# Performance work log

Hardware: AMD Instinct MI355X
Metric: run time of the kernel (lower is better)

## Reference

```python
import jax, jax.numpy as jnp
import numpy as np

# ---- static config (from search_space / module defaults) ----
B, NCG = 4096, 2                 # batch of archs, cell groups
NUM_INIT, NUM_NODE_INPUTS, NUM_STEPS = 2, 2, 4
NUM_NODES = NUM_INIT + NUM_STEPS  # 6
N_EDGE = NUM_NODE_INPUTS * NUM_STEPS  # 8
NUM_OPS = 7                      # 'none' is index 0
NONE_INDEX = 0
NODE_DIM = OP_DIM = HIDDEN = 48
GCN_DIMS = [128, 128]


def _uniform(key, shape, fan_in):
    s = 1.0 / np.sqrt(fan_in)
    return jax.random.uniform(key, shape, minval=-s, maxval=s, dtype=jnp.float32)


def setup_inputs() -> dict:
    key = jax.random.key(0)
    ks = jax.random.split(key, 14)
    # from-node for step i must be < NUM_INIT + i -> per-edge maxval [2,2,3,3,4,4,5,5]
    fmax = jnp.repeat(jnp.arange(NUM_INIT, NUM_NODES), NUM_NODE_INPUTS)
    f_nodes = jax.random.randint(ks[0], (B, NCG, N_EDGE), 0, fmax)
    ops = jax.random.randint(ks[1], (B, NCG, N_EDGE), 0, NUM_OPS)
    archs = jnp.stack([f_nodes, ops], axis=2).astype(jnp.int32)  # (B,NCG,2,E)

    init_node_emb = jax.random.normal(ks[2], (NCG, NUM_INIT, NODE_DIM), dtype=jnp.float32)
    other_node_emb = jnp.zeros((NCG, 1, NODE_DIM), dtype=jnp.float32)  # zero-init, trainable
    # op embeddings; 'none' op (idx 0) is frozen zeros
    op_embs = jax.random.normal(ks[3], (NUM_OPS, OP_DIM), dtype=jnp.float32).at[NONE_INDEX].set(0.0)

    Wx = _uniform(ks[4], (NODE_DIM, HIDDEN), NODE_DIM)
    bx = _uniform(ks[5], (HIDDEN,), NODE_DIM)
    W1 = _uniform(ks[6], (HIDDEN, GCN_DIMS[0]), GCN_DIMS[0])
    Wa1 = _uniform(ks[7], (OP_DIM, GCN_DIMS[0]), OP_DIM)
    ba1 = _uniform(ks[8], (GCN_DIMS[0],), OP_DIM)
    W2 = _uniform(ks[9], (GCN_DIMS[0], GCN_DIMS[1]), GCN_DIMS[1])
    Wa2 = _uniform(ks[10], (OP_DIM, GCN_DIMS[1]), OP_DIM)
    ba2 = _uniform(ks[11], (GCN_DIMS[1],), OP_DIM)
    return {"archs": archs, "init_node_emb": init_node_emb, "other_node_emb": other_node_emb,
            "op_embs": op_embs, "Wx": Wx, "bx": bx, "W1": W1, "Wa1": Wa1, "ba1": ba1,
            "W2": W2, "Wa2": Wa2, "ba2": ba2}


def _build_adj_ops(archs):
    """Dense adjacency (edge counts) and per-input-slot op-index matrices."""
    f = archs[:, :, 0, :].reshape(-1, N_EDGE)    # (B*NCG, E) from-nodes
    ops = archs[:, :, 1, :].reshape(-1, N_EDGE)  # (B*NCG, E) op ids
    t = jnp.repeat(jnp.arange(NUM_INIT, NUM_NODES), NUM_NODE_INPUTS)  # (E,) to-nodes
    Bt = B * NCG
    b_idx = jnp.arange(Bt)[:, None]
    adj = jnp.zeros((Bt, NUM_NODES, NUM_NODES), jnp.float32)
    adj = adj.at[b_idx, t[None, :], f].add(1.0)
    adj_op_inds = []
    for k in range(NUM_NODE_INPUTS):
        fk, tk, opk = f[:, k::NUM_NODE_INPUTS], t[k::NUM_NODE_INPUTS], ops[:, k::NUM_NODE_INPUTS]
        aoi = jnp.full((Bt, NUM_NODES, NUM_NODES), NONE_INDEX, dtype=jnp.int32)
        aoi = aoi.at[b_idx, tk[None, :], fk].set(opk)  # (t,f) unique within a slot
        adj_op_inds.append(aoi.reshape(B, NCG, NUM_NODES, NUM_NODES))
    return adj.reshape(B, NCG, NUM_NODES, NUM_NODES), adj_op_inds


def _gcn_layer(y, adj_op_inds, op_embs, W, Wa, ba):
    """DenseGraphOpEdgeFlow (defaults: attention, no plus_I/normalize/bias):
    out_i = support_i + sum_slots sum_j sigmoid(att(op_emb[op_ij])) * 1[op_ij != none] * support_j
    """
    support = y @ W                                   # (B,CG,N,out)
    out = support
    for aoi in adj_op_inds:
        attn = jax.nn.sigmoid(op_embs[aoi] @ Wa + ba)  # (B,CG,N,N,out)
        attn = attn * (aoi != NONE_INDEX)[..., None].astype(support.dtype)
        out = out + jnp.einsum('bcijo,bcjo->bcio', attn, support)
    return out


def reference(archs, init_node_emb, other_node_emb, op_embs, Wx, bx,
              W1, Wa1, ba1, W2, Wa2, ba2):
    _adj, adj_op_inds = _build_adj_ops(archs)  # adj counts unused under default gcn_kwargs
    node = jnp.concatenate([
        jnp.broadcast_to(init_node_emb[None], (B, NCG, NUM_INIT, NODE_DIM)),
        jnp.broadcast_to(other_node_emb[None], (B, NCG, NUM_STEPS, NODE_DIM))], axis=2)
    y = node @ Wx + bx                                 # x_hidden
    y = _gcn_layer(y, adj_op_inds, op_embs, W1, Wa1, ba1)
    y = jax.nn.relu(y)                                 # relu between layers
    y = _gcn_layer(y, adj_op_inds, op_embs, W2, Wa2, ba2)
    y = y[:, :, NUM_INIT:, :].mean(axis=2)             # drop init nodes, mean over steps
    return y.reshape(B, -1)                            # (B, NCG*128)
```

## Files before the change

kernel.cpp:

```cpp
#include <hip/hip_runtime.h>

#define NPAIR 8192

#define WS_S1   0
#define WS_AT1  1536
#define WS_AT2  2432
#define WS_S2I  3328

__device__ __forceinline__ float sigmoidf_(float x) {
  return 1.0f / (1.0f + __expf(-x));
}

__global__ __launch_bounds__(512) void precompute_kernel(
    const float* __restrict__ init_emb, const float* __restrict__ other_emb,
    const float* __restrict__ op_embs,  const float* __restrict__ Wx,
    const float* __restrict__ bx,       const float* __restrict__ W1,
    const float* __restrict__ Wa1,      const float* __restrict__ ba1,
    const float* __restrict__ W2,       const float* __restrict__ Wa2,
    const float* __restrict__ ba2,      float* __restrict__ ws)
{
  const int t   = threadIdx.x;
  const int blk = blockIdx.x;

  __shared__ float y0[2 * 6 * 48];
  __shared__ float s1sh[2 * 6 * 128];

  for (int idx = t; idx < 2 * 6 * 48; idx += 512) {
    int c = idx / 288, i = (idx / 48) % 6, h = idx % 48;
    const float* nptr = (i < 2) ? (init_emb + (c * 2 + i) * 48)
                                : (other_emb + c * 48);
    float acc = bx[h];
    for (int d = 0; d < 48; ++d)
      acc += nptr[d] * Wx[d * 48 + h];
    y0[idx] = acc;
  }
  __syncthreads();

  for (int idx = t; idx < 2 * 6 * 128; idx += 512) {
    int ci = idx >> 7, o = idx & 127;
    const float* yp = y0 + ci * 48;
    float acc = 0.f;
    for (int h = 0; h < 48; ++h) acc += yp[h] * W1[h * 128 + o];
    s1sh[idx] = acc;
    ws[WS_S1 + idx] = acc;
  }

  for (int idx = blk * 112 + t; idx < (blk + 1) * 112; idx += 512) {
    int op = idx >> 7, o = idx & 127;
    float a1 = ba1[o], a2 = ba2[o];
    for (int d = 0; d < 48; ++d) {
      float e = op_embs[op * 48 + d];
      a1 += e * Wa1[d * 128 + o];
      a2 += e * Wa2[d * 128 + o];
    }
    ws[WS_AT1 + idx] = (op == 0) ? 0.f : sigmoidf_(a1);
    ws[WS_AT2 + idx] = (op == 0) ? 0.f : sigmoidf_(a2);
  }
  __syncthreads();

  for (int idx = blk * 64 + t; idx < (blk + 1) * 64; idx += 512) {
    int c = idx >> 8, i = (idx >> 7) & 1, o = idx & 127;
    const float* sp = s1sh + (c * 6 + i) * 128;
    float acc = 0.f;
    for (int h = 0; h < 128; ++h)
      acc += fmaxf(sp[h], 0.f) * W2[h * 128 + o];
    ws[WS_S2I + idx] = acc;
  }
}

#define COMP4(v, j) ((j) == 0 ? (v).x : (j) == 1 ? (v).y : (j) == 2 ? (v).z : (v).w)

__global__ __launch_bounds__(256) void main_kernel(
    const int* __restrict__ archs, const float* __restrict__ W2,
    const float* __restrict__ ws, float* __restrict__ out)
{
  const int t  = threadIdx.x;
  const int pp = t >> 6;
  const int o2 = t & 63;
  const int P  = blockIdx.x * 4 + pp;
  const int c  = P & 1;

  __shared__ float w2sh[8192];
  __shared__ float y1sh[4][512];
  __shared__ int   archsh[64];
  if (t < 64) archsh[t] = archs[blockIdx.x * 64 + t];
  __syncthreads();

  int f[8], op[8];
  #pragma unroll
  for (int e = 0; e < 8; ++e) { f[e] = archsh[pp * 16 + e]; op[e] = archsh[pp * 16 + 8 + e]; }

  const float2* s1p = (const float2*)ws + c * 384;
  const float2* at1 = (const float2*)(ws + WS_AT1);
  const float2* at2 = (const float2*)(ws + WS_AT2);
  const float2* s2i = (const float2*)(ws + WS_S2I) + c * 128;

  float2 A2[8];
  #pragma unroll
  for (int e = 0; e < 8; ++e) A2[e] = at2[op[e] * 64 + o2];
  float2 S0 = s2i[o2], S1 = s2i[64 + o2];

  #pragma unroll
  for (int i = 0; i < 4; ++i) {
    float2 v = s1p[(2 + i) * 64 + o2];
    int e0 = 2 * i, e1 = 2 * i + 1;
    float2 A0 = at1[op[e0] * 64 + o2];
    float2 B0 = s1p[f[e0] * 64 + o2];
    float2 A1 = at1[op[e1] * 64 + o2];
    float2 B1 = s1p[f[e1] * 64 + o2];
    v.x += A0.x * B0.x + A1.x * B1.x;
    v.y += A0.y * B0.y + A1.y * B1.y;
    ((float2*)(y1sh[pp] + i * 128))[o2] =
        make_float2(fmaxf(v.x, 0.f), fmaxf(v.y, 0.f));
  }

  const float* y1p = y1sh[pp];
  float ax0 = 0, ax1 = 0, ax2 = 0, ax3 = 0;
  float ay0 = 0, ay1 = 0, ay2 = 0, ay3 = 0;

  for (int half = 0; half < 2; ++half) {
    __syncthreads();
    #pragma unroll
    for (int k = 0; k < 8; ++k)
      ((float4*)w2sh)[t + k * 256] = ((const float4*)W2)[half * 2048 + t + k * 256];
    __syncthreads();

    const float2* w2f = (const float2*)w2sh;
    const float*  yh  = y1p + half * 64;
    for (int h = 0; h < 64; h += 4) {
      float4 q0 = *(const float4*)(yh + 0 * 128 + h);
      float4 q1 = *(const float4*)(yh + 1 * 128 + h);
      float4 q2 = *(const float4*)(yh + 2 * 128 + h);
      float4 q3 = *(const float4*)(yh + 3 * 128 + h);
      #pragma unroll
      for (int j = 0; j < 4; ++j) {
        float2 wf = w2f[(h + j) * 64 + o2];
        float w0 = wf.x, w1 = wf.y, y;
        y = COMP4(q0, j); ax0 += y * w0; ay0 += y * w1;
        y = COMP4(q1, j); ax1 += y * w0; ay1 += y * w1;
        y = COMP4(q2, j); ax2 += y * w0; ay2 += y * w1;
        y = COMP4(q3, j); ax3 += y * w0; ay3 += y * w1;
      }
    }
  }

  float r0 = ax0 + ax1 + ax2 + ax3;
  float r1 = ay0 + ay1 + ay2 + ay3;
  #pragma unroll
  for (int e = 0; e < 8; ++e) {
    int fe = f[e];
    float sx, sy;
    if (fe == 0)      { sx = S0.x; sy = S0.y; }
    else if (fe == 1) { sx = S1.x; sy = S1.y; }
    else if (fe == 2) { sx = ax0; sy = ay0; }
    else if (fe == 3) { sx = ax1; sy = ay1; }
    else if (fe == 4) { sx = ax2; sy = ay2; }
    else              { sx = ax3; sy = ay3; }
    r0 += A2[e].x * sx;
    r1 += A2[e].y * sy;
  }
  r0 *= 0.25f; r1 *= 0.25f;

  ((float2*)out)[P * 64 + o2] = make_float2(r0, r1);
}

extern "C" void kernel_launch(void* const* d_in, const int* in_sizes, int n_in,
                              void* d_out, int out_size, void* d_ws, size_t ws_size,
                              hipStream_t stream) {
  const int* archs = (const int*)d_in[0];
  float* ws = (float*)d_ws;
  precompute_kernel<<<8, 512, 0, stream>>>(
      (const float*)d_in[1], (const float*)d_in[2], (const float*)d_in[3],
      (const float*)d_in[4], (const float*)d_in[5], (const float*)d_in[6],
      (const float*)d_in[7], (const float*)d_in[8], (const float*)d_in[9],
      (const float*)d_in[10], (const float*)d_in[11], ws);
  main_kernel<<<NPAIR / 4, 256, 0, stream>>>(archs, (const float*)d_in[9], ws,
                                             (float*)d_out);
}
```

Baseline: 121.3 us.

## Precompute second-layer support for all node configurations and gather per arch

Each intermediate node's first-layer output depends only on its two (from-node, op) inputs and the cell group. The new path enumerates all 5292 possible configurations, computes their layer-2 support (y1 @ W2) once in a config kernel, and stores them in a workspace table. The per-arch kernel then only gathers four table rows plus the attention terms, removing the per-arch 128x128 matmul. The old path stays as a fallback when the workspace is too small, and it now reads W2 directly from global memory instead of staging it in shared memory.

```diff
diff --git a/kernel.cpp b/kernel.cpp
--- a/kernel.cpp
+++ b/kernel.cpp
@@ -2,14 +2,195 @@
 
 #define NPAIR 8192
 
-#define WS_S1   0
-#define WS_AT1  1536
-#define WS_AT2  2432
-#define WS_S2I  3328
+#define NCFG_REAL 5292
+#define NCFG      5296
+#define CPER      2646
+#define WS_AT2F   0
+#define WS_TAB    1024
+#define WS_NEED   ((size_t)(1024 + NCFG * 128) * 4)
+
+#define COMP4(v, j) ((j) == 0 ? (v).x : (j) == 1 ? (v).y : (j) == 2 ? (v).z : (v).w)
 
 __device__ __forceinline__ float sigmoidf_(float x) {
   return 1.0f / (1.0f + __expf(-x));
 }
+
+__global__ __launch_bounds__(512) void config_kernel(
+    const float* __restrict__ init_emb, const float* __restrict__ other_emb,
+    const float* __restrict__ op_embs,  const float* __restrict__ Wx,
+    const float* __restrict__ bx,       const float* __restrict__ W1,
+    const float* __restrict__ Wa1,      const float* __restrict__ ba1,
+    const float* __restrict__ W2,       const float* __restrict__ Wa2,
+    const float* __restrict__ ba2,      float* __restrict__ ws)
+{
+  __shared__ float y0[576];
+  __shared__ float s1sh[1536];
+  __shared__ float at1sh[896];
+  __shared__ float at2sh[896];
+  __shared__ float y1sh[8192];
+  const int t = threadIdx.x;
+
+  for (int idx = t; idx < 576; idx += 512) {
+    int c = idx / 288, i = (idx / 48) % 6, h = idx % 48;
+    const float* nptr = (i < 2) ? (init_emb + (c * 2 + i) * 48)
+                                : (other_emb + c * 48);
+    float acc = bx[h];
+    for (int d = 0; d < 48; ++d) acc += nptr[d] * Wx[d * 48 + h];
+    y0[idx] = acc;
+  }
+  for (int idx = t; idx < 896; idx += 512) {
+    int op = idx >> 7, o = idx & 127;
+    float a1 = ba1[o], a2 = ba2[o];
+    for (int d = 0; d < 48; ++d) {
+      float e = op_embs[op * 48 + d];
+      a1 += e * Wa1[d * 128 + o];
+      a2 += e * Wa2[d * 128 + o];
+    }
+    float v1 = (op == 0) ? 0.f : sigmoidf_(a1);
+    float v2 = (op == 0) ? 0.f : sigmoidf_(a2);
+    at1sh[idx] = v1;
+    at2sh[idx] = v2;
+    ws[WS_AT2F + idx] = v2;
+  }
+  __syncthreads();
+  for (int idx = t; idx < 1536; idx += 512) {
+    int ci = idx >> 7, o = idx & 127;
+    const float* yp = y0 + ci * 48;
+    float acc = 0.f;
+    for (int h = 0; h < 48; ++h) acc += yp[h] * W1[h * 128 + o];
+    s1sh[idx] = acc;
+  }
+  __syncthreads();
+
+  const int w  = t >> 6, o2 = t & 63;
+  const int cfg0 = (blockIdx.x * 8 + w) * 8;
+  const float2* s1f = (const float2*)s1sh;
+  const float2* a1f = (const float2*)at1sh;
+
+  #pragma unroll
+  for (int r = 0; r < 8; ++r) {
+    int cfg = cfg0 + r;
+    if (cfg >= NCFG) continue;
+    float2 v;
+    if (cfg < NCFG_REAL) {
+      int c = cfg / CPER, q = cfg % CPER;
+      int i, b;
+      if (q < 196)       { i = 2; b = 0; }
+      else if (q < 637)  { i = 3; b = 196; }
+      else if (q < 1421) { i = 4; b = 637; }
+      else               { i = 5; b = 1421; }
+      q -= b;
+      int op2_ = q % 7; q /= 7;
+      int f2_  = q % i; q /= i;
+      int op1_ = q % 7;
+      int f1_  = q / 7;
+      int cb = c * 384;
+      v = s1f[cb + i * 64 + o2];
+      float2 A0 = a1f[op1_ * 64 + o2], B0 = s1f[cb + f1_ * 64 + o2];
+      float2 A1 = a1f[op2_ * 64 + o2], B1 = s1f[cb + f2_ * 64 + o2];
+      v.x += A0.x * B0.x + A1.x * B1.x;
+      v.y += A0.y * B0.y + A1.y * B1.y;
+    } else {
+      int j = cfg - NCFG_REAL, c = j >> 1, i = j & 1;
+      v = s1f[c * 384 + i * 64 + o2];
+    }
+    ((float2*)(y1sh + (w * 8 + r) * 128))[o2] =
+        make_float2(fmaxf(v.x, 0.f), fmaxf(v.y, 0.f));
+  }
+  __syncthreads();
+
+  const float* yb = y1sh + (w * 8) * 128;
+  const float2* W2f = (const float2*)W2;
+  float2 acc[8];
+  #pragma unroll
+  for (int r = 0; r < 8; ++r) acc[r] = make_float2(0.f, 0.f);
+
+  for (int k = 0; k < 128; k += 4) {
+    float4 yv[8];
+    #pragma unroll
+    for (int r = 0; r < 8; ++r)
+      yv[r] = *(const float4*)(yb + r * 128 + k);
+    #pragma unroll
+    for (int j = 0; j < 4; ++j) {
+      float2 wv = W2f[(k + j) * 64 + o2];
+      #pragma unroll
+      for (int r = 0; r < 8; ++r) {
+        float y = COMP4(yv[r], j);
+        acc[r].x += y * wv.x;
+        acc[r].y += y * wv.y;
+      }
+    }
+  }
+
+  float2* tab = (float2*)(ws + WS_TAB);
+  #pragma unroll
+  for (int r = 0; r < 8; ++r) {
+    int cfg = cfg0 + r;
+    if (cfg < NCFG) tab[cfg * 64 + o2] = acc[r];
+  }
+}
+
+__global__ __launch_bounds__(256) void gather_kernel(
+    const int* __restrict__ archs, const float* __restrict__ ws,
+    float* __restrict__ out)
+{
+  const int t  = threadIdx.x;
+  const int pp = t >> 6;
+  const int o2 = t & 63;
+  const int P  = blockIdx.x * 4 + pp;
+  const int c  = P & 1;
+
+  __shared__ int archsh[64];
+  if (t < 64) archsh[t] = archs[blockIdx.x * 64 + t];
+  __syncthreads();
+
+  int f[8], op[8];
+  #pragma unroll
+  for (int e = 0; e < 8; ++e) { f[e] = archsh[pp * 16 + e]; op[e] = archsh[pp * 16 + 8 + e]; }
+
+  const float2* tab = (const float2*)(ws + WS_TAB);
+  const float2* a2f = (const float2*)(ws + WS_AT2F);
+
+  float2 S0 = tab[(NCFG_REAL + c * 2 + 0) * 64 + o2];
+  float2 S1 = tab[(NCFG_REAL + c * 2 + 1) * 64 + o2];
+  float2 S2, S3, S4, S5;
+  {
+    const int ib[4] = {0, 196, 637, 1421};
+    #pragma unroll
+    for (int i = 2; i < 6; ++i) {
+      int e0 = 2 * (i - 2), e1 = e0 + 1;
+      int cid = c * CPER + ib[i - 2] +
+                ((f[e0] * 7 + op[e0]) * i + f[e1]) * 7 + op[e1];
+      float2 v = tab[cid * 64 + o2];
+      if (i == 2) S2 = v; else if (i == 3) S3 = v;
+      else if (i == 4) S4 = v; else S5 = v;
+    }
+  }
+  float2 A2[8];
+  #pragma unroll
+  for (int e = 0; e < 8; ++e) A2[e] = a2f[op[e] * 64 + o2];
+
+  float r0 = S2.x + S3.x + S4.x + S5.x;
+  float r1 = S2.y + S3.y + S4.y + S5.y;
+  #pragma unroll
+  for (int e = 0; e < 8; ++e) {
+    int fe = f[e];
+    float sx, sy;
+    if (fe == 0)      { sx = S0.x; sy = S0.y; }
+    else if (fe == 1) { sx = S1.x; sy = S1.y; }
+    else if (fe == 2) { sx = S2.x; sy = S2.y; }
+    else if (fe == 3) { sx = S3.x; sy = S3.y; }
+    else              { sx = S4.x; sy = S4.y; }
+    r0 += A2[e].x * sx;
+    r1 += A2[e].y * sy;
+  }
+  ((float2*)out)[P * 64 + o2] = make_float2(r0 * 0.25f, r1 * 0.25f);
+}
+
+#define FB_S1   0
+#define FB_AT1  1536
+#define FB_AT2  2432
+#define FB_S2I  3328
 
 __global__ __launch_bounds__(512) void precompute_kernel(
     const float* __restrict__ init_emb, const float* __restrict__ other_emb,
@@ -21,30 +202,25 @@
 {
   const int t   = threadIdx.x;
   const int blk = blockIdx.x;
-
-  __shared__ float y0[2 * 6 * 48];
-  __shared__ float s1sh[2 * 6 * 128];
-
-  for (int idx = t; idx < 2 * 6 * 48; idx += 512) {
+  __shared__ float y0[576];
+  __shared__ float s1sh[1536];
+  for (int idx = t; idx < 576; idx += 512) {
     int c = idx / 288, i = (idx / 48) % 6, h = idx % 48;
     const float* nptr = (i < 2) ? (init_emb + (c * 2 + i) * 48)
                                 : (other_emb + c * 48);
     float acc = bx[h];
-    for (int d = 0; d < 48; ++d)
-      acc += nptr[d] * Wx[d * 48 + h];
+    for (int d = 0; d < 48; ++d) acc += nptr[d] * Wx[d * 48 + h];
     y0[idx] = acc;
   }
   __syncthreads();
-
-  for (int idx = t; idx < 2 * 6 * 128; idx += 512) {
+  for (int idx = t; idx < 1536; idx += 512) {
     int ci = idx >> 7, o = idx & 127;
     const float* yp = y0 + ci * 48;
     float acc = 0.f;
     for (int h = 0; h < 48; ++h) acc += yp[h] * W1[h * 128 + o];
     s1sh[idx] = acc;
-    ws[WS_S1 + idx] = acc;
-  }
-
+    ws[FB_S1 + idx] = acc;
+  }
   for (int idx = blk * 112 + t; idx < (blk + 1) * 112; idx += 512) {
     int op = idx >> 7, o = idx & 127;
     float a1 = ba1[o], a2 = ba2[o];
@@ -53,22 +229,18 @@
       a1 += e * Wa1[d * 128 + o];
       a2 += e * Wa2[d * 128 + o];
     }
-    ws[WS_AT1 + idx] = (op == 0) ? 0.f : sigmoidf_(a1);
-    ws[WS_AT2 + idx] = (op == 0) ? 0.f : sigmoidf_(a2);
-  }
-  __syncthreads();
-
+    ws[FB_AT1 + idx] = (op == 0) ? 0.f : sigmoidf_(a1);
+    ws[FB_AT2 + idx] = (op == 0) ? 0.f : sigmoidf_(a2);
+  }
+  __syncthreads();
   for (int idx = blk * 64 + t; idx < (blk + 1) * 64; idx += 512) {
     int c = idx >> 8, i = (idx >> 7) & 1, o = idx & 127;
     const float* sp = s1sh + (c * 6 + i) * 128;
     float acc = 0.f;
-    for (int h = 0; h < 128; ++h)
-      acc += fmaxf(sp[h], 0.f) * W2[h * 128 + o];
-    ws[WS_S2I + idx] = acc;
-  }
-}
-
-#define COMP4(v, j) ((j) == 0 ? (v).x : (j) == 1 ? (v).y : (j) == 2 ? (v).z : (v).w)
+    for (int h = 0; h < 128; ++h) acc += fmaxf(sp[h], 0.f) * W2[h * 128 + o];
+    ws[FB_S2I + idx] = acc;
+  }
+}
 
 __global__ __launch_bounds__(256) void main_kernel(
     const int* __restrict__ archs, const float* __restrict__ W2,
@@ -79,27 +251,21 @@
   const int o2 = t & 63;
   const int P  = blockIdx.x * 4 + pp;
   const int c  = P & 1;
-
-  __shared__ float w2sh[8192];
   __shared__ float y1sh[4][512];
   __shared__ int   archsh[64];
   if (t < 64) archsh[t] = archs[blockIdx.x * 64 + t];
   __syncthreads();
-
   int f[8], op[8];
   #pragma unroll
   for (int e = 0; e < 8; ++e) { f[e] = archsh[pp * 16 + e]; op[e] = archsh[pp * 16 + 8 + e]; }
-
   const float2* s1p = (const float2*)ws + c * 384;
-  const float2* at1 = (const float2*)(ws + WS_AT1);
-  const float2* at2 = (const float2*)(ws + WS_AT2);
-  const float2* s2i = (const float2*)(ws + WS_S2I) + c * 128;
-
+  const float2* at1 = (const float2*)(ws + FB_AT1);
+  const float2* at2 = (const float2*)(ws + FB_AT2);
+  const float2* s2i = (const float2*)(ws + FB_S2I) + c * 128;
   float2 A2[8];
   #pragma unroll
   for (int e = 0; e < 8; ++e) A2[e] = at2[op[e] * 64 + o2];
   float2 S0 = s2i[o2], S1 = s2i[64 + o2];
-
   #pragma unroll
   for (int i = 0; i < 4; ++i) {
     float2 v = s1p[(2 + i) * 64 + o2];
@@ -113,37 +279,26 @@
     ((float2*)(y1sh[pp] + i * 128))[o2] =
         make_float2(fmaxf(v.x, 0.f), fmaxf(v.y, 0.f));
   }
-
+  __syncthreads();
   const float* y1p = y1sh[pp];
+  const float2* W2f = (const float2*)W2;
   float ax0 = 0, ax1 = 0, ax2 = 0, ax3 = 0;
   float ay0 = 0, ay1 = 0, ay2 = 0, ay3 = 0;
-
-  for (int half = 0; half < 2; ++half) {
-    __syncthreads();
+  for (int h = 0; h < 128; h += 4) {
+    float4 q0 = *(const float4*)(y1p + 0 * 128 + h);
+    float4 q1 = *(const float4*)(y1p + 1 * 128 + h);
+    float4 q2 = *(const float4*)(y1p + 2 * 128 + h);
+    float4 q3 = *(const float4*)(y1p + 3 * 128 + h);
     #pragma unroll
-    for (int k = 0; k < 8; ++k)
-      ((float4*)w2sh)[t + k * 256] = ((const float4*)W2)[half * 2048 + t + k * 256];
-    __syncthreads();
-
-    const float2* w2f = (const float2*)w2sh;
-    const float*  yh  = y1p + half * 64;
-    for (int h = 0; h < 64; h += 4) {
-      float4 q0 = *(const float4*)(yh + 0 * 128 + h);
-      float4 q1 = *(const float4*)(yh + 1 * 128 + h);
-      float4 q2 = *(const float4*)(yh + 2 * 128 + h);
-      float4 q3 = *(const float4*)(yh + 3 * 128 + h);
-      #pragma unroll
-      for (int j = 0; j < 4; ++j) {
-        float2 wf = w2f[(h + j) * 64 + o2];
-        float w0 = wf.x, w1 = wf.y, y;
-        y = COMP4(q0, j); ax0 += y * w0; ay0 += y * w1;
-        y = COMP4(q1, j); ax1 += y * w0; ay1 += y * w1;
-        y = COMP4(q2, j); ax2 += y * w0; ay2 += y * w1;
-        y = COMP4(q3, j); ax3 += y * w0; ay3 += y * w1;
-      }
-    }
-  }
-
+    for (int j = 0; j < 4; ++j) {
+      float2 wf = W2f[(h + j) * 64 + o2];
+      float w0 = wf.x, w1 = wf.y, y;
+      y = COMP4(q0, j); ax0 += y * w0; ay0 += y * w1;
+      y = COMP4(q1, j); ax1 += y * w0; ay1 += y * w1;
+      y = COMP4(q2, j); ax2 += y * w0; ay2 += y * w1;
+      y = COMP4(q3, j); ax3 += y * w0; ay3 += y * w1;
+    }
+  }
   float r0 = ax0 + ax1 + ax2 + ax3;
   float r1 = ay0 + ay1 + ay2 + ay3;
   #pragma unroll
@@ -159,9 +314,7 @@
     r0 += A2[e].x * sx;
     r1 += A2[e].y * sy;
   }
-  r0 *= 0.25f; r1 *= 0.25f;
-
-  ((float2*)out)[P * 64 + o2] = make_float2(r0, r1);
+  ((float2*)out)[P * 64 + o2] = make_float2(r0 * 0.25f, r1 * 0.25f);
 }
 
 extern "C" void kernel_launch(void* const* d_in, const int* in_sizes, int n_in,
@@ -169,11 +322,20 @@
                               hipStream_t stream) {
   const int* archs = (const int*)d_in[0];
   float* ws = (float*)d_ws;
-  precompute_kernel<<<8, 512, 0, stream>>>(
-      (const float*)d_in[1], (const float*)d_in[2], (const float*)d_in[3],
-      (const float*)d_in[4], (const float*)d_in[5], (const float*)d_in[6],
-      (const float*)d_in[7], (const float*)d_in[8], (const float*)d_in[9],
-      (const float*)d_in[10], (const float*)d_in[11], ws);
-  main_kernel<<<NPAIR / 4, 256, 0, stream>>>(archs, (const float*)d_in[9], ws,
-                                             (float*)d_out);
-}
+  if (ws_size >= WS_NEED) {
+    config_kernel<<<83, 512, 0, stream>>>(
+        (const float*)d_in[1], (const float*)d_in[2], (const float*)d_in[3],
+        (const float*)d_in[4], (const float*)d_in[5], (const float*)d_in[6],
+        (const float*)d_in[7], (const float*)d_in[8], (const float*)d_in[9],
+        (const float*)d_in[10], (const float*)d_in[11], ws);
+    gather_kernel<<<NPAIR / 4, 256, 0, stream>>>(archs, ws, (float*)d_out);
+  } else {
+    precompute_kernel<<<8, 512, 0, stream>>>(
+        (const float*)d_in[1], (const float*)d_in[2], (const float*)d_in[3],
+        (const float*)d_in[4], (const float*)d_in[5], (const float*)d_in[6],
+        (const float*)d_in[7], (const float*)d_in[8], (const float*)d_in[9],
+        (const float*)d_in[10], (const float*)d_in[11], ws);
+    main_kernel<<<NPAIR / 4, 256, 0, stream>>>(archs, (const float*)d_in[9], ws,
+                                               (float*)d_out);
+  }
+}
```

Measured after the change: 106.0 us. 12.6% less time.
